# Optimization experiments

Hardware: AMD Instinct MI355X
Metric: run time of the kernel (lower is better)

The kernel has to match this reference:

```python
import jax, jax.numpy as jnp
from jax import lax
import numpy as np

B, CIN, H, W = 32, 3, 128, 128
HID = 256          # hidden_dim == embedding_dim
K = 512            # num_embeddings
CC = 0.25          # commitment_cost
RR = 16            # SE reduction ratio


def setup_inputs() -> dict:
    key = jax.random.key(0)
    ks = iter(jax.random.split(key, 40))
    def n(shape, s=0.05):
        return jax.random.normal(next(ks), shape, jnp.float32) * s
    inp = {"x": jax.random.normal(next(ks), (B, CIN, H, W), jnp.float32)}
    inp.update(
        ec1_w=n((HID, CIN, 4, 4)), ec1_b=n((HID,)),
        ec2_w=n((HID, HID, 2, 2)), ec2_b=n((HID,)),
        se1_w1=n((HID // RR, HID)), se1_b1=n((HID // RR,)), se1_w2=n((HID, HID // RR)), se1_b2=n((HID,)), sa1_w=n((1, 2, 7, 7)),
        se2_w1=n((HID // RR, HID)), se2_b1=n((HID // RR,)), se2_w2=n((HID, HID // RR)), se2_b2=n((HID,)), sa2_w=n((1, 2, 7, 7)),
        codebook=jax.random.uniform(next(ks), (K, HID), jnp.float32, -1.0 / K, 1.0 / K),
        dt1_w=n((HID, HID, 2, 2)), dt1_b=n((HID,)),
        dt2_w=n((HID, CIN, 4, 4)), dt2_b=n((CIN,)),
        dse_w1=n((HID // RR, HID)), dse_b1=n((HID // RR,)), dse_w2=n((HID, HID // RR)), dse_b2=n((HID,)), dsa_w=n((2, 1, 7, 7)),
    )
    return inp


def conv(x, w, b, stride, pad=0):
    y = lax.conv_general_dilated(x, w, (stride, stride), [(pad, pad), (pad, pad)],
                                 dimension_numbers=('NCHW', 'OIHW', 'NCHW'))
    return y if b is None else y + b[None, :, None, None]


def convt(x, w, b, stride, pad=0):
    # torch ConvTranspose2d(weight [Cin, Cout, kh, kw]) == conv with flipped kernel,
    # lhs dilated by stride, padding k-1-pad
    k = w.shape[2]
    p = k - 1 - pad
    y = lax.conv_general_dilated(x, jnp.flip(w, (2, 3)), (1, 1), [(p, p), (p, p)],
                                 lhs_dilation=(stride, stride),
                                 dimension_numbers=('NCHW', 'IOHW', 'NCHW'))
    return y if b is None else y + b[None, :, None, None]


def se(x, w1, b1, w2, b2):
    s = jnp.mean(x, (2, 3))                                   # [B, C] global avg pool
    g = jax.nn.sigmoid(jax.nn.relu(s @ w1.T + b1) @ w2.T + b2)
    return x * g[:, :, None, None]


def cbam(x, w1, b1, w2, b2, sw, transpose=False):
    out = se(x, w1, b1, w2, b2)
    cat = jnp.concatenate([jnp.mean(out, 1, keepdims=True), jnp.max(out, 1, keepdims=True)], 1)
    s = convt(cat, sw, None, 1, 3) if transpose else conv(cat, sw, None, 1, 3)
    out = out * jax.nn.sigmoid(s)
    return x * out  # note: original CBAM.forward multiplies by x again


def vq(z, cb):
    D = cb.shape[1]
    flat = z.reshape(-1, D)  # faithful to torch reshape(-1, embedding_dim) on NCHW
    # squared euclidean distances (argmin identical to cdist argmin)
    d2 = jnp.sum(flat * flat, 1, keepdims=True) - 2.0 * (flat @ cb.T) + jnp.sum(cb * cb, 1)
    idx = jnp.argmin(d2, 1)
    q = cb[idx].reshape(z.shape)  # == one_hot(idx) @ cb, without materializing one-hot
    e_loss = jnp.mean((lax.stop_gradient(q) - z) ** 2)
    q_loss = jnp.mean((q - lax.stop_gradient(z)) ** 2)
    loss = q_loss + CC * e_loss
    q_st = z + lax.stop_gradient(q - z)
    p = jnp.zeros((cb.shape[0],), z.dtype).at[idx].add(1.0) / flat.shape[0]
    perplexity = jnp.exp(-jnp.sum(p * jnp.log(p + 1e-10)))
    return loss, q_st, perplexity


def reference(x, ec1_w, ec1_b, ec2_w, ec2_b,
              se1_w1, se1_b1, se1_w2, se1_b2, sa1_w,
              se2_w1, se2_b1, se2_w2, se2_b2, sa2_w,
              codebook, dt1_w, dt1_b, dt2_w, dt2_b,
              dse_w1, dse_b1, dse_w2, dse_b2, dsa_w):
    # encoder
    h = cbam(jax.nn.relu(conv(x, ec1_w, ec1_b, 2)), se1_w1, se1_b1, se1_w2, se1_b2, sa1_w)
    z = cbam(jax.nn.relu(conv(h, ec2_w, ec2_b, 1)), se2_w1, se2_b1, se2_w2, se2_b2, sa2_w)
    # vector quantization
    loss, q, perplexity = vq(z, codebook)
    # decoder
    d = cbam(jax.nn.relu(convt(q, dt1_w, dt1_b, 1)), dse_w1, dse_b1, dse_w2, dse_b2, dsa_w, transpose=True)
    x_recon = convt(d, dt2_w, dt2_b, 2)
    return x_recon, loss, perplexity
```

## Files before the change

### kernel.cpp

```cpp
#include <hip/hip_runtime.h>
#include <math.h>

#define NB 32
#define HID 256
#define HW1 (63*63)
#define HW2 (62*62)
#define T63 ((size_t)NB*HID*HW1)
#define T62 ((size_t)NB*HID*HW2)
#define NROWS 123008
#define KCB 512
#define GATHER_BLOCKS 1024

typedef __attribute__((ext_vector_type(8))) short short8;
typedef __attribute__((ext_vector_type(4))) float f32x4;
typedef __attribute__((ext_vector_type(4))) unsigned short us4;

__device__ __forceinline__ unsigned short f2bf(float f) {
    union { float f; unsigned int u; } v; v.f = f;
    unsigned int u = v.u;
    return (unsigned short)((u + 0x7FFFu + ((u >> 16) & 1u)) >> 16);
}
__device__ __forceinline__ float bf2f(unsigned short u) {
    union { unsigned int i; float f; } v; v.i = ((unsigned int)u) << 16;
    return v.f;
}

__global__ __launch_bounds__(256) void zero_small(float* __restrict__ sse, int* __restrict__ counts) {
    if (threadIdx.x == 0) sse[0] = 0.f;
    for (int i = threadIdx.x; i < KCB; i += 256) counts[i] = 0;
}
__global__ __launch_bounds__(256) void zero_pooled(float* __restrict__ pooled) {
    pooled[blockIdx.x*256 + threadIdx.x] = 0.f;
}

__global__ __launch_bounds__(256) void prepack_c1(
    const float* __restrict__ w, unsigned short* __restrict__ pack) {
    int t = blockIdx.x*256 + threadIdx.x;
    if (t >= 16384) return;
    int j = t & 7, lk = (t >> 3) & 3, co = (t >> 5) & 255, kc = t >> 13;
    int k = kc*32 + lk*8 + j;
    pack[t] = (k < 48) ? f2bf(w[co*48 + k]) : (unsigned short)0;
}

__global__ __launch_bounds__(256) void conv1_mfma(
    const float* __restrict__ x, const unsigned short* __restrict__ apack,
    const float* __restrict__ bias, unsigned short* __restrict__ X0) {
    __shared__ float xs[3][18][18];
    __shared__ __align__(16) unsigned short Bm[64*72];
    int b = blockIdx.y, t = blockIdx.x;
    int oh0 = (t >> 3)*8, ow0 = (t & 7)*8;
    int ih0 = oh0*2, iw0 = ow0*2;
    const float* xb = x + (size_t)b*3*128*128;
    for (int i = threadIdx.x; i < 972; i += 256) {
        int c = i / 324, rem = i - c*324, r = rem / 18, cl = rem - r*18;
        int ih = ih0 + r, iw = iw0 + cl;
        xs[c][r][cl] = (ih < 128 && iw < 128) ? xb[((size_t)c*128 + ih)*128 + iw] : 0.f;
    }
    __syncthreads();
    for (int i = threadIdx.x; i < 2048; i += 256) {
        int px = i >> 5, kp = (i & 31)*2;
        int ph = px >> 3, pw = px & 7;
        unsigned int pk = 0;
        #pragma unroll
        for (int u = 0; u < 2; ++u) {
            int k = kp + u;
            float v = 0.f;
            if (k < 48) {
                int c = k >> 4, k2 = k & 15, kh = k2 >> 2, kw = k2 & 3;
                v = xs[c][ph*2+kh][pw*2+kw];
            }
            pk |= ((unsigned int)f2bf(v)) << (16*u);
        }
        *(unsigned int*)&Bm[px*72 + kp] = pk;
    }
    __syncthreads();

    int w = threadIdx.x >> 6, l = threadIdx.x & 63;
    int lr = l & 15, lk = l >> 4;
    f32x4 acc[4][4];
    #pragma unroll
    for (int i = 0; i < 4; ++i)
        #pragma unroll
        for (int j = 0; j < 4; ++j) acc[i][j] = (f32x4){0.f,0.f,0.f,0.f};

    #pragma unroll
    for (int kc = 0; kc < 2; ++kc) {
        short8 bf[4];
        #pragma unroll
        for (int pxf = 0; pxf < 4; ++pxf)
            bf[pxf] = *(const short8*)&Bm[(pxf*16+lr)*72 + kc*32 + lk*8];
        #pragma unroll
        for (int cof = 0; cof < 4; ++cof) {
            int co = w*64 + cof*16 + lr;
            short8 af = *(const short8*)(apack + (((size_t)kc*256 + co)*4 + (size_t)lk)*8);
            acc[cof][0] = __builtin_amdgcn_mfma_f32_16x16x32_bf16(af, bf[0], acc[cof][0], 0, 0, 0);
            acc[cof][1] = __builtin_amdgcn_mfma_f32_16x16x32_bf16(af, bf[1], acc[cof][1], 0, 0, 0);
            acc[cof][2] = __builtin_amdgcn_mfma_f32_16x16x32_bf16(af, bf[2], acc[cof][2], 0, 0, 0);
            acc[cof][3] = __builtin_amdgcn_mfma_f32_16x16x32_bf16(af, bf[3], acc[cof][3], 0, 0, 0);
        }
    }
    #pragma unroll
    for (int cof = 0; cof < 4; ++cof) {
        int cob = w*64 + cof*16 + lk*4;
        float4 bz = *(const float4*)&bias[cob];
        #pragma unroll
        for (int pxf = 0; pxf < 4; ++pxf) {
            int px = pxf*16 + lr;
            int oh = oh0 + (px >> 3), ow = ow0 + (px & 7);
            if (oh < 63 && ow < 63) {
                f32x4 a = acc[cof][pxf];
                us4 pk = { f2bf(fmaxf(a.x + bz.x, 0.f)), f2bf(fmaxf(a.y + bz.y, 0.f)),
                           f2bf(fmaxf(a.z + bz.z, 0.f)), f2bf(fmaxf(a.w + bz.w, 0.f)) };
                *(us4*)(X0 + ((size_t)b*HW1 + (size_t)oh*63 + ow)*256 + cob) = pk;
            }
        }
    }
}

__global__ __launch_bounds__(256) void gap_nhwc(
    const unsigned short* __restrict__ X, float* __restrict__ pooled,
    int HW, float inv) {
    int b = blockIdx.y;
    int px0 = blockIdx.x * 512;
    int o = threadIdx.x & 31, pg = threadIdx.x >> 5;
    const unsigned short* xb = X + (size_t)b*HW*256 + o*8;
    float acc[8];
    #pragma unroll
    for (int j = 0; j < 8; ++j) acc[j] = 0.f;
    for (int i = 0; i < 64; ++i) {
        int px = px0 + pg + i*8;
        if (px < HW) {
            short8 v = *(const short8*)(xb + (size_t)px*256);
            #pragma unroll
            for (int j = 0; j < 8; ++j) acc[j] += bf2f((unsigned short)v[j]);
        }
    }
    __shared__ float pool2[8][256];
    #pragma unroll
    for (int j = 0; j < 8; ++j) pool2[pg][o*8+j] = acc[j];
    __syncthreads();
    float s = 0.f;
    #pragma unroll
    for (int p = 0; p < 8; ++p) s += pool2[p][threadIdx.x];
    atomicAdd(pooled + b*256 + threadIdx.x, s * inv);
}

__global__ __launch_bounds__(256) void gap_z(
    const unsigned short* __restrict__ Z, float* __restrict__ pooled, int HW) {
    int bc = blockIdx.x;
    const unsigned int* p = (const unsigned int*)(Z + (size_t)bc*HW);
    int n2 = HW >> 1;
    float s = 0.f;
    for (int i = threadIdx.x; i < n2; i += 256) {
        unsigned int v = p[i];
        s += bf2f((unsigned short)(v & 0xffff)) + bf2f((unsigned short)(v >> 16));
    }
    __shared__ float lds[4];
    for (int off = 32; off; off >>= 1) s += __shfl_down(s, off, 64);
    if ((threadIdx.x & 63) == 0) lds[threadIdx.x >> 6] = s;
    __syncthreads();
    if (threadIdx.x == 0) pooled[bc] = (lds[0]+lds[1]+lds[2]+lds[3]) / (float)HW;
}

__global__ __launch_bounds__(256) void se_mlp(
    const float* __restrict__ pooled, const float* __restrict__ w1,
    const float* __restrict__ b1, const float* __restrict__ w2,
    const float* __restrict__ b2, float* __restrict__ g) {
    int b = blockIdx.x;
    __shared__ float ps[256], hs[16];
    ps[threadIdx.x] = pooled[b*256 + threadIdx.x];
    __syncthreads();
    if (threadIdx.x < 16) {
        float a = b1[threadIdx.x];
        const float* wr = w1 + threadIdx.x*256;
        for (int k = 0; k < 256; ++k) a = fmaf(ps[k], wr[k], a);
        hs[threadIdx.x] = fmaxf(a, 0.f);
    }
    __syncthreads();
    float a = b2[threadIdx.x];
    const float* wr = w2 + threadIdx.x*16;
    #pragma unroll
    for (int j = 0; j < 16; ++j) a = fmaf(hs[j], wr[j], a);
    g[b*256 + threadIdx.x] = 1.f / (1.f + expf(-a));
}

__global__ __launch_bounds__(256) void chanpool_nhwc(
    const unsigned short* __restrict__ X, const float* __restrict__ g,
    float* __restrict__ am, int HW) {
    int b = blockIdx.y;
    __shared__ float gs[256];
    gs[threadIdx.x] = g[b*256 + threadIdx.x];
    __syncthreads();
    int p = blockIdx.x*256 + threadIdx.x;
    if (p >= HW) return;
    const unsigned short* xp = X + ((size_t)b*HW + p)*256;
    float s = 0.f, mx = -3.0e38f;
    for (int o = 0; o < 32; ++o) {
        short8 v = *(const short8*)(xp + o*8);
        #pragma unroll
        for (int j = 0; j < 8; ++j) {
            float f = bf2f((unsigned short)v[j]) * gs[o*8+j];
            s += f; mx = fmaxf(mx, f);
        }
    }
    am[((size_t)b*2)*HW + p]   = s * (1.f/256.f);
    am[((size_t)b*2+1)*HW + p] = mx;
}

__global__ __launch_bounds__(256) void chanpool_z(
    const unsigned short* __restrict__ Z, const float* __restrict__ g,
    float* __restrict__ am, int HW) {
    int b = blockIdx.y;
    __shared__ float gs[256];
    gs[threadIdx.x] = g[b*256 + threadIdx.x];
    __syncthreads();
    int p = blockIdx.x*256 + threadIdx.x;
    if (p >= HW) return;
    const unsigned short* xb = Z + (size_t)b*256*HW + p;
    float s = 0.f, mx = -3.0e38f;
    for (int c = 0; c < 256; ++c) {
        float v = bf2f(xb[(size_t)c*HW]) * gs[c];
        s += v; mx = fmaxf(mx, v);
    }
    am[((size_t)b*2)*HW + p]   = s * (1.f/256.f);
    am[((size_t)b*2+1)*HW + p] = mx;
}

__global__ __launch_bounds__(256) void spatial_conv(
    const float* __restrict__ am, const float* __restrict__ sw,
    float* __restrict__ ss, int H, int W, int transpose) {
    int b = blockIdx.y;
    int p = blockIdx.x*256 + threadIdx.x;
    __shared__ float ws[98];
    if (threadIdx.x < 98) {
        int c = threadIdx.x / 49, k = threadIdx.x % 49;
        int kh = k / 7, kw = k % 7;
        ws[threadIdx.x] = transpose ? sw[c*49 + (6-kh)*7 + (6-kw)]
                                    : sw[c*49 + kh*7 + kw];
    }
    __syncthreads();
    if (p >= H*W) return;
    int oh = p / W, ow = p % W;
    float acc = 0.f;
    #pragma unroll
    for (int c = 0; c < 2; ++c) {
        const float* ab = am + ((size_t)b*2 + c)*H*W;
        for (int kh = 0; kh < 7; ++kh) {
            int ih = oh + kh - 3;
            if (ih < 0 || ih >= H) continue;
            for (int kw = 0; kw < 7; ++kw) {
                int iw = ow + kw - 3;
                if (iw < 0 || iw >= W) continue;
                acc = fmaf(ab[(size_t)ih*W + iw], ws[c*49 + kh*7 + kw], acc);
            }
        }
    }
    ss[(size_t)b*H*W + p] = 1.f / (1.f + expf(-acc));
}

__global__ __launch_bounds__(256) void cbam_mul_nhwc(
    unsigned short* X, const float* __restrict__ g,
    const float* __restrict__ ss, int HW) {
    int b = blockIdx.y;
    __shared__ float gs[256];
    gs[threadIdx.x] = g[b*256 + threadIdx.x];
    __syncthreads();
    int p = blockIdx.x*256 + threadIdx.x;
    if (p >= HW) return;
    float sv = ss[(size_t)b*HW + p];
    unsigned short* xp = X + ((size_t)b*HW + p)*256;
    for (int o = 0; o < 32; ++o) {
        short8 v = *(const short8*)(xp + o*8);
        unsigned int pk[4];
        #pragma unroll
        for (int j = 0; j < 4; ++j) {
            float f0 = bf2f((unsigned short)v[2*j]);
            float f1 = bf2f((unsigned short)v[2*j+1]);
            f0 = f0*f0*gs[o*8+2*j]*sv;
            f1 = f1*f1*gs[o*8+2*j+1]*sv;
            pk[j] = (unsigned int)f2bf(f0) | ((unsigned int)f2bf(f1) << 16);
        }
        *(short8*)(xp + o*8) = *(const short8*)pk;
    }
}

__global__ __launch_bounds__(256) void cbam_z(
    unsigned short* Z, const float* __restrict__ g,
    const float* __restrict__ ss, int HW) {
    int b = blockIdx.y;
    int e2 = blockIdx.x*256 + threadIdx.x;
    if (e2 >= 128*HW) return;
    size_t e = (size_t)e2*2;
    int c = (int)(e / HW), p = (int)(e % HW);
    float gc = g[b*256 + c];
    float s0 = ss[(size_t)b*HW + p];
    float s1 = ss[(size_t)b*HW + p + 1];
    unsigned int* px = (unsigned int*)(Z + (size_t)b*256*HW + e);
    unsigned int v = *px;
    float f0 = bf2f((unsigned short)(v & 0xffff));
    float f1 = bf2f((unsigned short)(v >> 16));
    f0 = f0*f0*gc*s0;
    f1 = f1*f1*gc*s1;
    *px = (unsigned int)f2bf(f0) | ((unsigned int)f2bf(f1) << 16);
}

__global__ __launch_bounds__(256) void to_nhwc_bf16(
    const unsigned short* __restrict__ Z, unsigned short* __restrict__ X, int HW) {
    int b = blockIdx.y;
    int p = blockIdx.x*256 + threadIdx.x;
    bool valid = p < HW;
    const unsigned short* inb = Z + (size_t)b*256*HW + p;
    unsigned short* dst = X + ((size_t)b*HW + p)*256;
    #pragma unroll
    for (int ch = 0; ch < 4; ++ch) {
        unsigned short buf[64];
        #pragma unroll
        for (int j = 0; j < 64; ++j)
            buf[j] = valid ? inb[(size_t)(ch*64 + j)*HW] : (unsigned short)0;
        if (valid) {
            #pragma unroll
            for (int j2 = 0; j2 < 8; ++j2)
                *(short8*)(dst + ch*64 + j2*8) = *(const short8*)&buf[j2*8];
        }
    }
}

__global__ __launch_bounds__(256) void prepack_w(
    const float* __restrict__ w, unsigned short* __restrict__ pack, int transpose_flip) {
    int t = blockIdx.x*256 + threadIdx.x;
    int j = t & 7, koct = (t >> 3) & 3, co = (t >> 5) & 255, tap = (t >> 13) & 3, cc = t >> 15;
    int ci = cc*32 + koct*8 + j;
    int kh = tap >> 1, kw = tap & 1;
    float v;
    if (transpose_flip) v = w[((size_t)ci*256 + co)*4 + (1-kh)*2 + (1-kw)];
    else                v = w[((size_t)co*256 + ci)*4 + kh*2 + kw];
    pack[t] = f2bf(v);
}

__global__ __launch_bounds__(256) void prepack_dt2b(
    const float* __restrict__ w, unsigned short* __restrict__ pk) {
    int t = blockIdx.x*256 + threadIdx.x;
    int jj = t & 7, lk = (t >> 3) & 3, co = (t >> 5) & 15, j = (t >> 9) & 3, cc = (t >> 11) & 7, p = t >> 14;
    int ci = cc*32 + lk*8 + jj;
    int kh0 = p >> 1, kw0 = p & 1;
    const int dj[4] = {0, 2, 8, 10};
    float v = 0.f;
    if (co < 3) v = w[(size_t)ci*48 + co*16 + kh0*4 + kw0 + dj[j]];
    pk[t] = f2bf(v);
}

template <int MODE>
__global__ __launch_bounds__(256) void convk2_mfma_nhwc(
    const unsigned short* __restrict__ Xin, const unsigned short* __restrict__ apack,
    const float* __restrict__ bias, unsigned short* __restrict__ outZ,
    unsigned short* __restrict__ outU,
    int inH, int inW, int outH, int outW, int pad) {
    __shared__ __align__(16) unsigned short Sh[MODE ? 16896 : 6800];
    unsigned short* Ir0 = Sh;
    unsigned short* Ir1 = Sh + 3400;
    int b = blockIdx.y;
    int t = blockIdx.x;
    int oh0 = (t >> 2) * 4, ow0 = (t & 3) * 16;
    int w = threadIdx.x >> 6, l = threadIdx.x & 63;
    int lr = l & 15, lk = l >> 4;
    const unsigned short* src = Xin + (size_t)b*inH*inW*256;

    f32x4 acc[4][4];
    #pragma unroll
    for (int i = 0; i < 4; ++i)
        #pragma unroll
        for (int j = 0; j < 4; ++j) acc[i][j] = (f32x4){0.f,0.f,0.f,0.f};

    auto STAGE = [&](int cc, int bufi) {
        unsigned short* Ib = bufi ? Ir1 : Ir0;
        #pragma unroll
        for (int pass = 0; pass < 2; ++pass) {
            int u = pass*256 + threadIdx.x;
            if (u < 340) {
                int sp = u >> 2, q = u & 3;
                int r = (sp*241) >> 12, c = sp - r*17;
                int gh = oh0 + r - pad, gw = ow0 + c - pad;
                short8 v = (short8){0,0,0,0,0,0,0,0};
                if (gh >= 0 && gh < inH && gw >= 0 && gw < inW)
                    v = *(const short8*)(src + ((size_t)gh*inW + gw)*256 + cc*32 + q*8);
                *(short8*)&Ib[sp*40 + q*8] = v;
            }
        }
    };

    STAGE(0, 0);
    for (int cc = 0; cc < 8; ++cc) {
        __syncthreads();
        if (cc < 7) STAGE(cc+1, (cc+1)&1);
        const unsigned short* Ib = (cc & 1) ? Ir1 : Ir0;
        #pragma unroll
        for (int tap = 0; tap < 4; ++tap) {
            int kh = tap >> 1, kw = tap & 1;
            int spb = kh*17 + kw + lr;
            short8 b0 = *(const short8*)&Ib[(spb     )*40 + lk*8];
            short8 b1 = *(const short8*)&Ib[(spb + 17)*40 + lk*8];
            short8 b2 = *(const short8*)&Ib[(spb + 34)*40 + lk*8];
            short8 b3 = *(const short8*)&Ib[(spb + 51)*40 + lk*8];
            const unsigned short* abase = apack + (((size_t)(cc*4 + tap)*256)*4 + (size_t)lk)*8;
            #pragma unroll
            for (int cof = 0; cof < 4; ++cof) {
                int co = w*64 + cof*16 + lr;
                short8 af = *(const short8*)(abase + (size_t)co*32);
                acc[cof][0] = __builtin_amdgcn_mfma_f32_16x16x32_bf16(af, b0, acc[cof][0], 0, 0, 0);
                acc[cof][1] = __builtin_amdgcn_mfma_f32_16x16x32_bf16(af, b1, acc[cof][1], 0, 0, 0);
                acc[cof][2] = __builtin_amdgcn_mfma_f32_16x16x32_bf16(af, b2, acc[cof][2], 0, 0, 0);
                acc[cof][3] = __builtin_amdgcn_mfma_f32_16x16x32_bf16(af, b3, acc[cof][3], 0, 0, 0);
            }
        }
    }
    if (MODE == 0) {
        int ow = ow0 + lr;
        #pragma unroll
        for (int cof = 0; cof < 4; ++cof) {
            int cob = w*64 + cof*16 + lk*4;
            float4 bz = *(const float4*)&bias[cob];
            #pragma unroll
            for (int pxf = 0; pxf < 4; ++pxf) {
                int oh = oh0 + pxf;
                if (oh < outH && ow < outW) {
                    f32x4 a = acc[cof][pxf];
                    size_t base = ((size_t)(b*256 + cob)*outH + oh)*outW + ow;
                    size_t st = (size_t)outH*outW;
                    outZ[base]        = f2bf(fmaxf(a.x + bz.x, 0.f));
                    outZ[base +   st] = f2bf(fmaxf(a.y + bz.y, 0.f));
                    outZ[base + 2*st] = f2bf(fmaxf(a.z + bz.z, 0.f));
                    outZ[base + 3*st] = f2bf(fmaxf(a.w + bz.w, 0.f));
                }
            }
        }
    } else {
        __syncthreads();
        #pragma unroll
        for (int cof = 0; cof < 4; ++cof) {
            int cob = w*64 + cof*16 + lk*4;
            float4 bz = *(const float4*)&bias[cob];
            #pragma unroll
            for (int pxf = 0; pxf < 4; ++pxf) {
                f32x4 a = acc[cof][pxf];
                us4 pk = { f2bf(fmaxf(a.x + bz.x, 0.f)), f2bf(fmaxf(a.y + bz.y, 0.f)),
                           f2bf(fmaxf(a.z + bz.z, 0.f)), f2bf(fmaxf(a.w + bz.w, 0.f)) };
                *(us4*)&Sh[(pxf*16 + lr)*264 + cob] = pk;
            }
        }
        __syncthreads();
        int owp = threadIdx.x >> 4, c0 = (threadIdx.x & 15)*16;
        int ow = ow0 + owp;
        #pragma unroll
        for (int row = 0; row < 4; ++row) {
            int oh = oh0 + row;
            if (oh < outH && ow < outW) {
                unsigned short* dst = outU + (((size_t)b*outH + oh)*outW + ow)*256 + c0;
                *(short8*)dst       = *(const short8*)&Sh[(row*16 + owp)*264 + c0];
                *(short8*)(dst + 8) = *(const short8*)&Sh[(row*16 + owp)*264 + c0 + 8];
            }
        }
    }
}

__global__ __launch_bounds__(256) void cb_norm(
    const float* __restrict__ cb, float* __restrict__ cbn) {
    for (int n = threadIdx.x; n < KCB; n += 256) {
        float s = 0.f;
        for (int k = 0; k < 256; ++k) { float v = cb[(size_t)n*256+k]; s = fmaf(v,v,s); }
        cbn[n] = s;
    }
}

__global__ __launch_bounds__(256) void cb_pack(
    const float* __restrict__ cb, unsigned short* __restrict__ cbp) {
    int t = blockIdx.x*256 + threadIdx.x;
    cbp[t] = f2bf(cb[t]);
}

__global__ __launch_bounds__(256) void vq_assign_mfma(
    const unsigned short* __restrict__ z, const unsigned short* __restrict__ cbp,
    const float* __restrict__ cbn, int* __restrict__ idx) {
    __shared__ __align__(16) unsigned short zb[64*264];
    __shared__ __align__(16) unsigned short cbs[2][32*264];
    __shared__ float cbl[KCB];
    int r0 = blockIdx.x * 64;
    for (int v = threadIdx.x; v < 2048; v += 256) {
        int row = v >> 5, o = v & 31;
        *(short8*)&zb[row*264 + o*8] = *(const short8*)&z[(size_t)(r0+row)*256 + o*8];
    }
    for (int i = threadIdx.x; i < KCB; i += 256) cbl[i] = cbn[i];
    int tcode = threadIdx.x >> 3, tk = threadIdx.x & 7;
    auto STAGE_CB = [&](int c, int bufi) {
        const unsigned short* src = cbp + ((size_t)(c*32 + tcode))*256 + tk*8;
        unsigned short* dst = &cbs[bufi][tcode*264 + tk*8];
        #pragma unroll
        for (int j = 0; j < 4; ++j)
            *(short8*)(dst + j*64) = *(const short8*)(src + j*64);
    };
    STAGE_CB(0, 0);
    __syncthreads();

    int w = threadIdx.x >> 6, l = threadIdx.x & 63;
    int lr = l & 15, lk = l >> 4;
    short8 afr[8];
    #pragma unroll
    for (int ks = 0; ks < 8; ++ks)
        afr[ks] = *(const short8*)&zb[(w*16 + lr)*264 + ks*32 + lk*8];

    float bd[4]; int bi[4];
    #pragma unroll
    for (int r = 0; r < 4; ++r) { bd[r] = 3.0e38f; bi[r] = 0; }

    for (int c = 0; c < 16; ++c) {
        if (c < 15) STAGE_CB(c+1, (c+1)&1);
        const unsigned short* Cb = cbs[c & 1];
        #pragma unroll
        for (int f = 0; f < 2; ++f) {
            f32x4 acc = (f32x4){0.f,0.f,0.f,0.f};
            #pragma unroll
            for (int ks = 0; ks < 8; ++ks) {
                short8 bfr = *(const short8*)&Cb[(f*16 + lr)*264 + ks*32 + lk*8];
                acc = __builtin_amdgcn_mfma_f32_16x16x32_bf16(afr[ks], bfr, acc, 0, 0, 0);
            }
            int n = c*32 + f*16 + lr;
            float cn = cbl[n];
            #pragma unroll
            for (int r = 0; r < 4; ++r) {
                float dist = fmaf(-2.f, acc[r], cn);
                if (dist < bd[r]) { bd[r] = dist; bi[r] = n; }
            }
        }
        __syncthreads();
    }
    #pragma unroll
    for (int r = 0; r < 4; ++r) {
        #pragma unroll
        for (int off = 1; off < 16; off <<= 1) {
            float od = __shfl_xor(bd[r], off, 64);
            int   oi = __shfl_xor(bi[r], off, 64);
            if (od < bd[r] || (od == bd[r] && oi < bi[r])) { bd[r] = od; bi[r] = oi; }
        }
    }
    if (lr == 0) {
        #pragma unroll
        for (int r = 0; r < 4; ++r)
            idx[r0 + w*16 + lk*4 + r] = bi[r];
    }
}

__global__ __launch_bounds__(256) void vq_gather(
    unsigned short* zq, const float* __restrict__ cb,
    const int* __restrict__ idx, float* __restrict__ sse, int* __restrict__ counts) {
    __shared__ int hist[KCB];
    for (int i = threadIdx.x; i < KCB; i += 256) hist[i] = 0;
    __syncthreads();
    float local = 0.f;
    for (int r = blockIdx.x; r < NROWS; r += GATHER_BLOCKS) {
        int id = idx[r];
        if (threadIdx.x == 0) atomicAdd(&hist[id], 1);
        float qv = cb[(size_t)id*256 + threadIdx.x];
        unsigned short* pz = zq + (size_t)r*256 + threadIdx.x;
        float zv = bf2f(*pz);
        *pz = f2bf(qv);
        float d = qv - zv;
        local = fmaf(d, d, local);
    }
    __shared__ float lds[4];
    for (int off = 32; off; off >>= 1) local += __shfl_down(local, off, 64);
    if ((threadIdx.x & 63) == 0) lds[threadIdx.x >> 6] = local;
    __syncthreads();
    if (threadIdx.x == 0) atomicAdd(sse, lds[0]+lds[1]+lds[2]+lds[3]);
    for (int i = threadIdx.x; i < KCB; i += 256) {
        int h = hist[i];
        if (h) atomicAdd(counts + i, h);
    }
}

__global__ __launch_bounds__(256) void vq_finalize(
    const float* __restrict__ sse, const int* __restrict__ counts,
    float* __restrict__ out) {
    __shared__ float lds[4];
    float h = 0.f;
    for (int n = threadIdx.x; n < KCB; n += 256) {
        float p = (float)counts[n] * (1.f/123008.f);
        h += p * logf(p + 1e-10f);
    }
    for (int off = 32; off; off >>= 1) h += __shfl_down(h, off, 64);
    if ((threadIdx.x & 63) == 0) lds[threadIdx.x >> 6] = h;
    __syncthreads();
    if (threadIdx.x == 0) {
        out[1572864] = 1.25f * sse[0] / 31490048.f;
        out[1572865] = expf(-(lds[0]+lds[1]+lds[2]+lds[3]));
    }
}

__global__ __launch_bounds__(256) void dt2_mfma(
    const unsigned short* __restrict__ Y, const unsigned short* __restrict__ apack,
    const float* __restrict__ bias, float* __restrict__ out) {
    __shared__ __align__(16) unsigned short Iraw[2][289*40];
    int b = blockIdx.y, t = blockIdx.x;
    int a0 = (t >> 2)*16, b0 = (t & 3)*16;
    int p = threadIdx.x >> 6;
    int l = threadIdx.x & 63;
    int lr = l & 15, lk = l >> 4;
    const unsigned short* src = Y + (size_t)b*HW1*256;

    auto STAGE = [&](int cc, int bufi) {
        #pragma unroll
        for (int pass = 0; pass < 5; ++pass) {
            int u = pass*256 + threadIdx.x;
            if (u < 1156) {
                int sp = u >> 2, q = u & 3;
                int r = (sp*241) >> 12, c = sp - r*17;
                int ia = a0 - 1 + r, ib = b0 - 1 + c;
                short8 v = (short8){0,0,0,0,0,0,0,0};
                if (ia >= 0 && ia < 63 && ib >= 0 && ib < 63)
                    v = *(const short8*)(src + ((size_t)ia*63 + ib)*256 + cc*32 + q*8);
                *(short8*)&Iraw[bufi][sp*40 + q*8] = v;
            }
        }
    };

    f32x4 acc[16];
    #pragma unroll
    for (int i = 0; i < 16; ++i) acc[i] = (f32x4){0.f,0.f,0.f,0.f};

    STAGE(0, 0);
    for (int cc = 0; cc < 8; ++cc) {
        __syncthreads();
        if (cc < 7) STAGE(cc+1, (cc+1)&1);
        const unsigned short* Ib = Iraw[cc & 1];
        #pragma unroll
        for (int j = 0; j < 4; ++j) {
            int jh = j >> 1, jw = j & 1;
            short8 af = *(const short8*)(apack +
                ((size_t)((p*8 + cc)*4 + j))*512 + lr*32 + lk*8);
            int sp0 = (1 - jh)*17 + (lr + 1 - jw);
            #pragma unroll
            for (int nf = 0; nf < 16; ++nf) {
                short8 bf = *(const short8*)&Ib[(sp0 + nf*17)*40 + lk*8];
                acc[nf] = __builtin_amdgcn_mfma_f32_16x16x32_bf16(af, bf, acc[nf], 0, 0, 0);
            }
        }
    }
    if (lk == 0) {
        int kh0 = p >> 1, kw0 = p & 1;
        float bz0 = bias[0], bz1 = bias[1], bz2 = bias[2];
        int wp = 2*(b0 + lr) + kw0;
        #pragma unroll
        for (int nf = 0; nf < 16; ++nf) {
            int h = 2*(a0 + nf) + kh0;
            size_t ob = (size_t)(b*3)*16384 + (size_t)h*128 + wp;
            out[ob]         = acc[nf].x + bz0;
            out[ob + 16384] = acc[nf].y + bz1;
            out[ob + 32768] = acc[nf].z + bz2;
        }
    }
}

extern "C" void kernel_launch(void* const* d_in, const int* in_sizes, int n_in,
                              void* d_out, int out_size, void* d_ws, size_t ws_size,
                              hipStream_t stream) {
    const float* x      = (const float*)d_in[0];
    const float* ec1_w  = (const float*)d_in[1];
    const float* ec1_b  = (const float*)d_in[2];
    const float* ec2_w  = (const float*)d_in[3];
    const float* ec2_b  = (const float*)d_in[4];
    const float* se1_w1 = (const float*)d_in[5];
    const float* se1_b1 = (const float*)d_in[6];
    const float* se1_w2 = (const float*)d_in[7];
    const float* se1_b2 = (const float*)d_in[8];
    const float* sa1_w  = (const float*)d_in[9];
    const float* se2_w1 = (const float*)d_in[10];
    const float* se2_b1 = (const float*)d_in[11];
    const float* se2_w2 = (const float*)d_in[12];
    const float* se2_b2 = (const float*)d_in[13];
    const float* sa2_w  = (const float*)d_in[14];
    const float* cbk    = (const float*)d_in[15];
    const float* dt1_w  = (const float*)d_in[16];
    const float* dt1_b  = (const float*)d_in[17];
    const float* dt2_w  = (const float*)d_in[18];
    const float* dt2_b  = (const float*)d_in[19];
    const float* dse_w1 = (const float*)d_in[20];
    const float* dse_b1 = (const float*)d_in[21];
    const float* dse_w2 = (const float*)d_in[22];
    const float* dse_b2 = (const float*)d_in[23];
    const float* dsa_w  = (const float*)d_in[24];
    float* out = (float*)d_out;

    unsigned short* Zb = (unsigned short*)d_ws;
    unsigned short* U0 = Zb + T62;
    unsigned short* U1 = U0 + T63;
    float* pooled = (float*)(U1 + T63);
    float* g      = pooled + 8192;
    float* am     = g + 8192;
    float* ssmap  = am + (size_t)NB*2*HW1;
    float* cbn    = ssmap + (size_t)NB*HW1;
    unsigned short* apackE = (unsigned short*)(cbn + 512);
    unsigned short* apackD = apackE + 262144;
    unsigned short* cbp    = apackD + 262144;
    unsigned short* apackC = cbp + 131072;
    unsigned short* apack2 = apackC + 16384;
    float* sse    = (float*)(apack2 + 65536);
    int*   counts = (int*)(sse + 1);
    int*   idx    = counts + 512;

    zero_small<<<1, 256, 0, stream>>>(sse, counts);
    prepack_w<<<1024, 256, 0, stream>>>(ec2_w, apackE, 0);
    prepack_w<<<1024, 256, 0, stream>>>(dt1_w, apackD, 1);
    prepack_c1<<<64, 256, 0, stream>>>(ec1_w, apackC);
    prepack_dt2b<<<256, 256, 0, stream>>>(dt2_w, apack2);
    cb_norm<<<1, 256, 0, stream>>>(cbk, cbn);
    cb_pack<<<512, 256, 0, stream>>>(cbk, cbp);

    conv1_mfma<<<dim3(64, NB), 256, 0, stream>>>(x, apackC, ec1_b, U0);
    zero_pooled<<<32, 256, 0, stream>>>(pooled);
    gap_nhwc<<<dim3(8, NB), 256, 0, stream>>>(U0, pooled, HW1, 1.f/HW1);
    se_mlp<<<NB, 256, 0, stream>>>(pooled, se1_w1, se1_b1, se1_w2, se1_b2, g);
    chanpool_nhwc<<<dim3(16, NB), 256, 0, stream>>>(U0, g, am, HW1);
    spatial_conv<<<dim3(16, NB), 256, 0, stream>>>(am, sa1_w, ssmap, 63, 63, 0);
    cbam_mul_nhwc<<<dim3(16, NB), 256, 0, stream>>>(U0, g, ssmap, HW1);

    convk2_mfma_nhwc<0><<<dim3(64, NB), 256, 0, stream>>>(U0, apackE, ec2_b, Zb, (unsigned short*)0, 63, 63, 62, 62, 0);
    gap_z<<<NB*256, 256, 0, stream>>>(Zb, pooled, HW2);
    se_mlp<<<NB, 256, 0, stream>>>(pooled, se2_w1, se2_b1, se2_w2, se2_b2, g);
    chanpool_z<<<dim3(16, NB), 256, 0, stream>>>(Zb, g, am, HW2);
    spatial_conv<<<dim3(16, NB), 256, 0, stream>>>(am, sa2_w, ssmap, 62, 62, 0);
    cbam_z<<<dim3(1922, NB), 256, 0, stream>>>(Zb, g, ssmap, HW2);

    vq_assign_mfma<<<NROWS/64, 256, 0, stream>>>(Zb, cbp, cbn, idx);
    vq_gather<<<GATHER_BLOCKS, 256, 0, stream>>>(Zb, cbk, idx, sse, counts);
    vq_finalize<<<1, 256, 0, stream>>>(sse, counts, out);
    to_nhwc_bf16<<<dim3(16, NB), 256, 0, stream>>>(Zb, U1, HW2);

    convk2_mfma_nhwc<1><<<dim3(64, NB), 256, 0, stream>>>(U1, apackD, dt1_b, (unsigned short*)0, U0, 62, 62, 63, 63, 1);
    zero_pooled<<<32, 256, 0, stream>>>(pooled);
    gap_nhwc<<<dim3(8, NB), 256, 0, stream>>>(U0, pooled, HW1, 1.f/HW1);
    se_mlp<<<NB, 256, 0, stream>>>(pooled, dse_w1, dse_b1, dse_w2, dse_b2, g);
    chanpool_nhwc<<<dim3(16, NB), 256, 0, stream>>>(U0, g, am, HW1);
    spatial_conv<<<dim3(16, NB), 256, 0, stream>>>(am, dsa_w, ssmap, 63, 63, 1);
    cbam_mul_nhwc<<<dim3(16, NB), 256, 0, stream>>>(U0, g, ssmap, HW1);

    dt2_mfma<<<dim3(16, NB), 256, 0, stream>>>(U0, apack2, dt2_b, out);
}
```

Before: 817.5 us.

## Retile 2x2 conv kernels to full-width two-row tiles with eight MFMA fragments

The 2x2 MFMA convolution now gives each block two full output rows (64 columns) instead of a 4x16 tile, staging a 3x65 input halo per channel chunk. Each A fragment loaded from the packed weights now feeds eight MFMAs instead of four, and halo overhead per output pixel drops. The transposed-mode epilogue writes NHWC directly from registers instead of going through shared memory. The cost is twice the accumulator registers (128 floats per thread), which can lower occupancy, plus uncoalesced 8-byte stores in the NHWC path.

```diff
diff --git a/kernel.cpp b/kernel.cpp
--- a/kernel.cpp
+++ b/kernel.cpp
@@ -355,35 +355,31 @@
     const float* __restrict__ bias, unsigned short* __restrict__ outZ,
     unsigned short* __restrict__ outU,
     int inH, int inW, int outH, int outW, int pad) {
-    __shared__ __align__(16) unsigned short Sh[MODE ? 16896 : 6800];
-    unsigned short* Ir0 = Sh;
-    unsigned short* Ir1 = Sh + 3400;
+    __shared__ __align__(16) unsigned short Iraw[2][195*40];
     int b = blockIdx.y;
-    int t = blockIdx.x;
-    int oh0 = (t >> 2) * 4, ow0 = (t & 3) * 16;
+    int oh0 = blockIdx.x * 2;
     int w = threadIdx.x >> 6, l = threadIdx.x & 63;
     int lr = l & 15, lk = l >> 4;
     const unsigned short* src = Xin + (size_t)b*inH*inW*256;
 
-    f32x4 acc[4][4];
+    f32x4 acc[4][8];
     #pragma unroll
     for (int i = 0; i < 4; ++i)
         #pragma unroll
-        for (int j = 0; j < 4; ++j) acc[i][j] = (f32x4){0.f,0.f,0.f,0.f};
+        for (int j = 0; j < 8; ++j) acc[i][j] = (f32x4){0.f,0.f,0.f,0.f};
 
     auto STAGE = [&](int cc, int bufi) {
-        unsigned short* Ib = bufi ? Ir1 : Ir0;
-        #pragma unroll
-        for (int pass = 0; pass < 2; ++pass) {
+        #pragma unroll
+        for (int pass = 0; pass < 4; ++pass) {
             int u = pass*256 + threadIdx.x;
-            if (u < 340) {
+            if (u < 780) {
                 int sp = u >> 2, q = u & 3;
-                int r = (sp*241) >> 12, c = sp - r*17;
-                int gh = oh0 + r - pad, gw = ow0 + c - pad;
+                int r = (sp*1009) >> 16, c = sp - r*65;
+                int gh = oh0 + r - pad, gw = c - pad;
                 short8 v = (short8){0,0,0,0,0,0,0,0};
                 if (gh >= 0 && gh < inH && gw >= 0 && gw < inW)
                     v = *(const short8*)(src + ((size_t)gh*inW + gw)*256 + cc*32 + q*8);
-                *(short8*)&Ib[sp*40 + q*8] = v;
+                *(short8*)&Iraw[bufi][sp*40 + q*8] = v;
             }
         }
     };
@@ -392,71 +388,52 @@
     for (int cc = 0; cc < 8; ++cc) {
         __syncthreads();
         if (cc < 7) STAGE(cc+1, (cc+1)&1);
-        const unsigned short* Ib = (cc & 1) ? Ir1 : Ir0;
+        const unsigned short* Ib = Iraw[cc & 1];
         #pragma unroll
         for (int tap = 0; tap < 4; ++tap) {
             int kh = tap >> 1, kw = tap & 1;
-            int spb = kh*17 + kw + lr;
-            short8 b0 = *(const short8*)&Ib[(spb     )*40 + lk*8];
-            short8 b1 = *(const short8*)&Ib[(spb + 17)*40 + lk*8];
-            short8 b2 = *(const short8*)&Ib[(spb + 34)*40 + lk*8];
-            short8 b3 = *(const short8*)&Ib[(spb + 51)*40 + lk*8];
+            short8 bf[8];
+            #pragma unroll
+            for (int r = 0; r < 2; ++r)
+                #pragma unroll
+                for (int q = 0; q < 4; ++q)
+                    bf[r*4+q] = *(const short8*)&Ib[((kh+r)*65 + kw + q*16 + lr)*40 + lk*8];
             const unsigned short* abase = apack + (((size_t)(cc*4 + tap)*256)*4 + (size_t)lk)*8;
             #pragma unroll
             for (int cof = 0; cof < 4; ++cof) {
                 int co = w*64 + cof*16 + lr;
                 short8 af = *(const short8*)(abase + (size_t)co*32);
-                acc[cof][0] = __builtin_amdgcn_mfma_f32_16x16x32_bf16(af, b0, acc[cof][0], 0, 0, 0);
-                acc[cof][1] = __builtin_amdgcn_mfma_f32_16x16x32_bf16(af, b1, acc[cof][1], 0, 0, 0);
-                acc[cof][2] = __builtin_amdgcn_mfma_f32_16x16x32_bf16(af, b2, acc[cof][2], 0, 0, 0);
-                acc[cof][3] = __builtin_amdgcn_mfma_f32_16x16x32_bf16(af, b3, acc[cof][3], 0, 0, 0);
-            }
-        }
-    }
-    if (MODE == 0) {
-        int ow = ow0 + lr;
-        #pragma unroll
-        for (int cof = 0; cof < 4; ++cof) {
-            int cob = w*64 + cof*16 + lk*4;
-            float4 bz = *(const float4*)&bias[cob];
-            #pragma unroll
-            for (int pxf = 0; pxf < 4; ++pxf) {
-                int oh = oh0 + pxf;
-                if (oh < outH && ow < outW) {
-                    f32x4 a = acc[cof][pxf];
+                #pragma unroll
+                for (int f = 0; f < 8; ++f)
+                    acc[cof][f] = __builtin_amdgcn_mfma_f32_16x16x32_bf16(af, bf[f], acc[cof][f], 0, 0, 0);
+            }
+        }
+    }
+    #pragma unroll
+    for (int cof = 0; cof < 4; ++cof) {
+        int cob = w*64 + cof*16 + lk*4;
+        float4 bz = *(const float4*)&bias[cob];
+        #pragma unroll
+        for (int f = 0; f < 8; ++f) {
+            int r = f >> 2, q = f & 3;
+            int oh = oh0 + r, ow = q*16 + lr;
+            if (oh < outH && ow < outW) {
+                f32x4 a = acc[cof][f];
+                float r0 = fmaxf(a.x + bz.x, 0.f);
+                float r1 = fmaxf(a.y + bz.y, 0.f);
+                float r2 = fmaxf(a.z + bz.z, 0.f);
+                float r3 = fmaxf(a.w + bz.w, 0.f);
+                if (MODE == 0) {
                     size_t base = ((size_t)(b*256 + cob)*outH + oh)*outW + ow;
                     size_t st = (size_t)outH*outW;
-                    outZ[base]        = f2bf(fmaxf(a.x + bz.x, 0.f));
-                    outZ[base +   st] = f2bf(fmaxf(a.y + bz.y, 0.f));
-                    outZ[base + 2*st] = f2bf(fmaxf(a.z + bz.z, 0.f));
-                    outZ[base + 3*st] = f2bf(fmaxf(a.w + bz.w, 0.f));
+                    outZ[base]        = f2bf(r0);
+                    outZ[base +   st] = f2bf(r1);
+                    outZ[base + 2*st] = f2bf(r2);
+                    outZ[base + 3*st] = f2bf(r3);
+                } else {
+                    us4 pk = { f2bf(r0), f2bf(r1), f2bf(r2), f2bf(r3) };
+                    *(us4*)(outU + (((size_t)b*outH + oh)*outW + ow)*256 + cob) = pk;
                 }
-            }
-        }
-    } else {
-        __syncthreads();
-        #pragma unroll
-        for (int cof = 0; cof < 4; ++cof) {
-            int cob = w*64 + cof*16 + lk*4;
-            float4 bz = *(const float4*)&bias[cob];
-            #pragma unroll
-            for (int pxf = 0; pxf < 4; ++pxf) {
-                f32x4 a = acc[cof][pxf];
-                us4 pk = { f2bf(fmaxf(a.x + bz.x, 0.f)), f2bf(fmaxf(a.y + bz.y, 0.f)),
-                           f2bf(fmaxf(a.z + bz.z, 0.f)), f2bf(fmaxf(a.w + bz.w, 0.f)) };
-                *(us4*)&Sh[(pxf*16 + lr)*264 + cob] = pk;
-            }
-        }
-        __syncthreads();
-        int owp = threadIdx.x >> 4, c0 = (threadIdx.x & 15)*16;
-        int ow = ow0 + owp;
-        #pragma unroll
-        for (int row = 0; row < 4; ++row) {
-            int oh = oh0 + row;
-            if (oh < outH && ow < outW) {
-                unsigned short* dst = outU + (((size_t)b*outH + oh)*outW + ow)*256 + c0;
-                *(short8*)dst       = *(const short8*)&Sh[(row*16 + owp)*264 + c0];
-                *(short8*)(dst + 8) = *(const short8*)&Sh[(row*16 + owp)*264 + c0 + 8];
             }
         }
     }
@@ -721,7 +698,7 @@
     spatial_conv<<<dim3(16, NB), 256, 0, stream>>>(am, sa1_w, ssmap, 63, 63, 0);
     cbam_mul_nhwc<<<dim3(16, NB), 256, 0, stream>>>(U0, g, ssmap, HW1);
 
-    convk2_mfma_nhwc<0><<<dim3(64, NB), 256, 0, stream>>>(U0, apackE, ec2_b, Zb, (unsigned short*)0, 63, 63, 62, 62, 0);
+    convk2_mfma_nhwc<0><<<dim3(31, NB), 256, 0, stream>>>(U0, apackE, ec2_b, Zb, (unsigned short*)0, 63, 63, 62, 62, 0);
     gap_z<<<NB*256, 256, 0, stream>>>(Zb, pooled, HW2);
     se_mlp<<<NB, 256, 0, stream>>>(pooled, se2_w1, se2_b1, se2_w2, se2_b2, g);
     chanpool_z<<<dim3(16, NB), 256, 0, stream>>>(Zb, g, am, HW2);
@@ -733,7 +710,7 @@
     vq_finalize<<<1, 256, 0, stream>>>(sse, counts, out);
     to_nhwc_bf16<<<dim3(16, NB), 256, 0, stream>>>(Zb, U1, HW2);
 
-    convk2_mfma_nhwc<1><<<dim3(64, NB), 256, 0, stream>>>(U1, apackD, dt1_b, (unsigned short*)0, U0, 62, 62, 63, 63, 1);
+    convk2_mfma_nhwc<1><<<dim3(32, NB), 256, 0, stream>>>(U1, apackD, dt1_b, (unsigned short*)0, U0, 62, 62, 63, 63, 1);
     zero_pooled<<<32, 256, 0, stream>>>(pooled);
     gap_nhwc<<<dim3(8, NB), 256, 0, stream>>>(U0, pooled, HW1, 1.f/HW1);
     se_mlp<<<NB, 256, 0, stream>>>(pooled, dse_w1, dse_b1, dse_w2, dse_b2, g);
```

Measured after the change: 1.112 ms. 36.0% more time.
